# Optimization experiments

Hardware: AMD Instinct MI355X
Metric: run time of the kernel (lower is better)

The kernel has to match this reference:

```python
import jax, jax.numpy as jnp
import numpy as np

N_NODES = 100000
N_EDGES = 1600000
HEADS = 4
HID = 64
IN_CH = 3
N_GRAPHS = 64
NEG_SLOPE = 0.2  # PyG GATConv default


def _gat_layer(x, src, dst, W, a_src, a_dst, b):
    """PyG GATConv with concat=False (head-mean), eval mode (no dropout)."""
    N = x.shape[0]
    xl = (x @ W).reshape(N, HEADS, HID)            # [N,H,C]
    es = (xl * a_src).sum(-1)                       # [N,H] alpha_src
    ed = (xl * a_dst).sum(-1)                       # [N,H] alpha_dst
    e = jax.nn.leaky_relu(es[src] + ed[dst], NEG_SLOPE)  # [E,H]
    # segment softmax over incoming edges of each dst node
    m = jax.ops.segment_max(e, dst, num_segments=N)      # [N,H]
    ex = jnp.exp(e - m[dst])
    s = jax.ops.segment_sum(ex, dst, num_segments=N)     # [N,H]
    alpha = ex / s[dst]                                   # [E,H]
    msg = xl[src] * alpha[:, :, None]                     # [E,H,C]
    out = jax.ops.segment_sum(msg, dst, num_segments=N)   # [N,H,C]
    return out.mean(axis=1) + b                            # head mean + bias


def setup_inputs() -> dict:
    key = jax.random.key(0)
    ks = jax.random.split(key, 12)
    x = jax.random.normal(ks[0], (N_NODES, IN_CH), dtype=jnp.float32)
    edge_index = jax.random.randint(ks[1], (2, N_EDGES), 0, N_NODES, dtype=jnp.int64)
    batch_ids = jnp.sort(jax.random.randint(ks[2], (N_NODES,), 0, N_GRAPHS, dtype=jnp.int64))
    def glorot(k, shape, fan_in):
        return jax.random.normal(k, shape, dtype=jnp.float32) / np.sqrt(fan_in)
    W1 = glorot(ks[3], (IN_CH, HEADS * HID), IN_CH)
    a_src1 = glorot(ks[4], (HEADS, HID), HID)
    a_dst1 = glorot(ks[5], (HEADS, HID), HID)
    b1 = jnp.zeros((HID,), dtype=jnp.float32)
    W2 = glorot(ks[6], (HID, HEADS * HID), HID)
    a_src2 = glorot(ks[7], (HEADS, HID), HID)
    a_dst2 = glorot(ks[8], (HEADS, HID), HID)
    b2 = jnp.zeros((HID,), dtype=jnp.float32)
    return {"x": x, "edge_index": edge_index, "batch_ids": batch_ids,
            "W1": W1, "a_src1": a_src1, "a_dst1": a_dst1, "b1": b1,
            "W2": W2, "a_src2": a_src2, "a_dst2": a_dst2, "b2": b2}


def reference(x, edge_index, batch_ids, W1, a_src1, a_dst1, b1, W2, a_src2, a_dst2, b2):
    src, dst = edge_index[0], edge_index[1]
    h = jax.nn.relu(_gat_layer(x, src, dst, W1, a_src1, a_dst1, b1))
    h = jax.nn.relu(_gat_layer(h, src, dst, W2, a_src2, a_dst2, b2))
    # global_add_pool
    g = jax.ops.segment_sum(h, batch_ids, num_segments=N_GRAPHS)  # [G, HID]
    return g
```

## Files before the change

### kernel.cpp

```cpp
#include <hip/hip_runtime.h>
#include <math.h>

#define HEADS 4
#define HID 64
#define BSHIFT 7
#define BWIDTH 128
#define CCAP 4096
#define DCHUNK 8192

typedef __attribute__((ext_vector_type(8))) short short8;
typedef __attribute__((ext_vector_type(4))) float f32x4;

__device__ __forceinline__ float lrelu(float x) { return x > 0.f ? x : 0.2f * x; }

__device__ __forceinline__ unsigned short bf16r(float f) {
    unsigned u = __float_as_uint(f);
    unsigned r = (u + 0x7FFFu + ((u >> 16) & 1u)) >> 16;
    return (unsigned short)r;
}
__device__ __forceinline__ float bf2f(unsigned short u) {
    return __uint_as_float(((unsigned)u) << 16);
}

__device__ __forceinline__ float wred_sum(float v) {
#pragma unroll
    for (int o = 32; o > 0; o >>= 1) v += __shfl_xor(v, o);
    return v;
}
__device__ __forceinline__ float red16_sum(float v) {
#pragma unroll
    for (int o = 8; o > 0; o >>= 1) v += __shfl_xor(v, o);
    return v;
}
__device__ __forceinline__ float red16_max(float v) {
#pragma unroll
    for (int o = 8; o > 0; o >>= 1) v = fmaxf(v, __shfl_xor(v, o));
    return v;
}

__global__ void k_binit(int* __restrict__ bcnt, int NBUCK) {
    int i = threadIdx.x;
    if (i < NBUCK) bcnt[i] = 0;
}

__global__ void k_bhist(const int* __restrict__ dstI, int* __restrict__ bcnt,
                        int E, int NBUCK) {
    __shared__ int h[1024];
    for (int i = threadIdx.x; i < NBUCK; i += 256) h[i] = 0;
    __syncthreads();
    int stride = gridDim.x * 256;
    for (int e = blockIdx.x * 256 + threadIdx.x; e < E; e += stride)
        atomicAdd(&h[dstI[e] >> BSHIFT], 1);
    __syncthreads();
    for (int i = threadIdx.x; i < NBUCK; i += 256)
        if (h[i]) atomicAdd(&bcnt[i], h[i]);
}

__global__ void k_bscan(const int* __restrict__ bcnt, int* __restrict__ bbase,
                        int* __restrict__ gcur, int* __restrict__ off,
                        int NBUCK, int N, int E) {
    __shared__ int lds[1024];
    int t = threadIdx.x;
    int v = (t < NBUCK) ? bcnt[t] : 0;
    lds[t] = v;
    __syncthreads();
    for (int s = 1; s < 1024; s <<= 1) {
        int u = (t >= s) ? lds[t - s] : 0;
        __syncthreads();
        lds[t] += u;
        __syncthreads();
    }
    if (t < NBUCK) {
        int b = lds[t] - v;
        bbase[t] = b;
        gcur[t] = b;
    }
    if (t == 0) { bbase[NBUCK] = E; off[N] = E; }
}

__global__ void k_bdist(const int* __restrict__ srcI, const int* __restrict__ dstI,
                        int* __restrict__ gcur, uint2* __restrict__ pairs,
                        int E, int NBUCK) {
    __shared__ int h[1024];
    __shared__ int cur[1024];
    for (int i = threadIdx.x; i < NBUCK; i += 1024) h[i] = 0;
    __syncthreads();
    int base = blockIdx.x * DCHUNK;
    int sr[8], dr[8];
#pragma unroll
    for (int k = 0; k < 8; k++) {
        int e = base + threadIdx.x + k * 1024;
        if (e < E) {
            sr[k] = srcI[e];
            dr[k] = dstI[e];
            atomicAdd(&h[dr[k] >> BSHIFT], 1);
        } else dr[k] = -1;
    }
    __syncthreads();
    for (int i = threadIdx.x; i < NBUCK; i += 1024)
        cur[i] = h[i] ? atomicAdd(&gcur[i], h[i]) : 0;
    __syncthreads();
#pragma unroll
    for (int k = 0; k < 8; k++) {
        if (dr[k] >= 0) {
            int b = dr[k] >> BSHIFT;
            int p = atomicAdd(&cur[b], 1);
            pairs[p] = make_uint2((unsigned)sr[k], (unsigned)dr[k]);
        }
    }
}

__global__ void k_bcsr(const uint2* __restrict__ pairs, const int* __restrict__ bbase,
                       int* __restrict__ off, int* __restrict__ csr, int N) {
    __shared__ int cnt[BWIDTH];
    __shared__ int scan[BWIDTH];
    __shared__ int cur[BWIDTH];
    __shared__ int stage[CCAP];
    int b = blockIdx.x;
    int nodeBase = b << BSHIFT;
    int nNodes = N - nodeBase;
    if (nNodes > BWIDTH) nNodes = BWIDTH;
    int e0 = bbase[b], e1 = bbase[b + 1];
    int ecnt = e1 - e0;
    if (threadIdx.x < BWIDTH) cnt[threadIdx.x] = 0;
    __syncthreads();
    for (int i = threadIdx.x; i < ecnt; i += 256)
        atomicAdd(&cnt[pairs[e0 + i].y - (unsigned)nodeBase], 1);
    __syncthreads();
    if (threadIdx.x < BWIDTH)
        scan[threadIdx.x] = (threadIdx.x < nNodes) ? cnt[threadIdx.x] : 0;
    __syncthreads();
    for (int s = 1; s < BWIDTH; s <<= 1) {
        int u = 0;
        if (threadIdx.x < BWIDTH && threadIdx.x >= s) u = scan[threadIdx.x - s];
        __syncthreads();
        if (threadIdx.x < BWIDTH) scan[threadIdx.x] += u;
        __syncthreads();
    }
    if (threadIdx.x < nNodes) {
        int ex = scan[threadIdx.x] - cnt[threadIdx.x];
        off[nodeBase + threadIdx.x] = e0 + ex;
        cur[threadIdx.x] = ex;
    }
    __syncthreads();
    for (int i = threadIdx.x; i < ecnt; i += 256) {
        uint2 pr = pairs[e0 + i];
        int l = atomicAdd(&cur[pr.y - (unsigned)nodeBase], 1);
        if (l < CCAP) stage[l] = (int)pr.x;
        else csr[e0 + l] = (int)pr.x;
    }
    __syncthreads();
    int lim = ecnt < CCAP ? ecnt : CCAP;
    for (int i = threadIdx.x; i < lim; i += 256) csr[e0 + i] = stage[i];
}

__global__ void k_prep(const float* __restrict__ W, const float* __restrict__ asrc,
                       const float* __restrict__ adst, float* __restrict__ p_src,
                       float* __restrict__ p_dst, int K) {
    int wid = (blockIdx.x * blockDim.x + threadIdx.x) >> 6;
    int lane = threadIdx.x & 63;
    int total = K * 4 * 2;
    if (wid >= total) return;
    int which = wid / (K * 4);
    int hk = wid % (K * 4);
    int h = hk / K, k = hk % K;
    const float* a = which ? adst : asrc;
    float v = W[(size_t)k * 256 + h * 64 + lane] * a[h * 64 + lane];
    v = wred_sum(v);
    if (lane == 0) (which ? p_dst : p_src)[h * K + k] = v;
}

__global__ void k_w2bt(const float* __restrict__ W2, unsigned short* __restrict__ W2bt) {
    int i = blockIdx.x * 256 + threadIdx.x;
    int c = i >> 8, kh = i & 255;
    int h = kh >> 6, kf = kh & 63;
    W2bt[i] = bf16r(W2[kf * 256 + h * 64 + c]);
}

__global__ void k_esed1(const float* __restrict__ x, const float* __restrict__ ps,
                        const float* __restrict__ pd, float* __restrict__ es,
                        float* __restrict__ ed, int N) {
    int n = blockIdx.x * blockDim.x + threadIdx.x;
    if (n >= N) return;
    float x0 = x[n * 3], x1 = x[n * 3 + 1], x2 = x[n * 3 + 2];
    float4 s, d;
    s.x = x0 * ps[0] + x1 * ps[1] + x2 * ps[2];
    s.y = x0 * ps[3] + x1 * ps[4] + x2 * ps[5];
    s.z = x0 * ps[6] + x1 * ps[7] + x2 * ps[8];
    s.w = x0 * ps[9] + x1 * ps[10] + x2 * ps[11];
    d.x = x0 * pd[0] + x1 * pd[1] + x2 * pd[2];
    d.y = x0 * pd[3] + x1 * pd[4] + x2 * pd[5];
    d.z = x0 * pd[6] + x1 * pd[7] + x2 * pd[8];
    d.w = x0 * pd[9] + x1 * pd[10] + x2 * pd[11];
    ((float4*)es)[n] = s;
    ((float4*)ed)[n] = d;
}

__global__ void k_agg1(const int* __restrict__ off, const int* __restrict__ csr,
                       const float* __restrict__ es, const float* __restrict__ ed,
                       const float* __restrict__ x, const float* __restrict__ W1,
                       const float* __restrict__ b1, const float* __restrict__ qs,
                       const float* __restrict__ qd, unsigned short* __restrict__ houtb,
                       float* __restrict__ es2, float* __restrict__ ed2, int N) {
    int grp = (blockIdx.x * blockDim.x + threadIdx.x) >> 4;
    int l = threadIdx.x & 15;
    int wid = grp;
    bool active = wid < N;
    int o0 = 0, deg = 0;
    float4 edv = make_float4(0.f, 0.f, 0.f, 0.f);
    if (active) {
        o0 = off[wid];
        deg = off[wid + 1] - o0;
        edv = ((const float4*)ed)[wid];
    }

    float m0 = -INFINITY, m1 = -INFINITY, m2 = -INFINITY, m3 = -INFINITY;
    int s_cache = 0;
    float c0 = 0.f, c1 = 0.f, c2 = 0.f, c3 = 0.f;
    for (int j = l; j < deg; j += 16) {
        int s = csr[o0 + j];
        float4 ev = ((const float4*)es)[s];
        float e0 = lrelu(ev.x + edv.x), e1 = lrelu(ev.y + edv.y);
        float e2 = lrelu(ev.z + edv.z), e3 = lrelu(ev.w + edv.w);
        if (j < 16) { s_cache = s; c0 = e0; c1 = e1; c2 = e2; c3 = e3; }
        m0 = fmaxf(m0, e0); m1 = fmaxf(m1, e1);
        m2 = fmaxf(m2, e2); m3 = fmaxf(m3, e3);
    }
    m0 = red16_max(m0); m1 = red16_max(m1); m2 = red16_max(m2); m3 = red16_max(m3);

    float t0 = 0.f, t1 = 0.f, t2 = 0.f, t3 = 0.f;
    for (int j = l; j < deg; j += 16) {
        float e0, e1, e2, e3;
        if (j < 16) { e0 = c0; e1 = c1; e2 = c2; e3 = c3; }
        else {
            int s = csr[o0 + j];
            float4 ev = ((const float4*)es)[s];
            e0 = lrelu(ev.x + edv.x); e1 = lrelu(ev.y + edv.y);
            e2 = lrelu(ev.z + edv.z); e3 = lrelu(ev.w + edv.w);
        }
        e0 = __expf(e0 - m0); e1 = __expf(e1 - m1);
        e2 = __expf(e2 - m2); e3 = __expf(e3 - m3);
        if (j < 16) { c0 = e0; c1 = e1; c2 = e2; c3 = e3; }
        t0 += e0; t1 += e1; t2 += e2; t3 += e3;
    }
    t0 = red16_sum(t0); t1 = red16_sum(t1); t2 = red16_sum(t2); t3 = red16_sum(t3);
    float i0 = t0 > 0.f ? 1.f / t0 : 0.f;
    float i1 = t1 > 0.f ? 1.f / t1 : 0.f;
    float i2 = t2 > 0.f ? 1.f / t2 : 0.f;
    float i3 = t3 > 0.f ? 1.f / t3 : 0.f;

    float a00 = 0, a01 = 0, a02 = 0, a10 = 0, a11 = 0, a12 = 0;
    float a20 = 0, a21 = 0, a22 = 0, a30 = 0, a31 = 0, a32 = 0;
    for (int j = l; j < deg; j += 16) {
        float e0, e1, e2, e3; int s;
        if (j < 16) { s = s_cache; e0 = c0; e1 = c1; e2 = c2; e3 = c3; }
        else {
            s = csr[o0 + j];
            float4 ev = ((const float4*)es)[s];
            e0 = __expf(lrelu(ev.x + edv.x) - m0);
            e1 = __expf(lrelu(ev.y + edv.y) - m1);
            e2 = __expf(lrelu(ev.z + edv.z) - m2);
            e3 = __expf(lrelu(ev.w + edv.w) - m3);
        }
        float xv0 = x[s * 3], xv1 = x[s * 3 + 1], xv2 = x[s * 3 + 2];
        a00 += e0 * xv0; a01 += e0 * xv1; a02 += e0 * xv2;
        a10 += e1 * xv0; a11 += e1 * xv1; a12 += e1 * xv2;
        a20 += e2 * xv0; a21 += e2 * xv1; a22 += e2 * xv2;
        a30 += e3 * xv0; a31 += e3 * xv1; a32 += e3 * xv2;
    }
    a00 = red16_sum(a00) * i0; a01 = red16_sum(a01) * i0; a02 = red16_sum(a02) * i0;
    a10 = red16_sum(a10) * i1; a11 = red16_sum(a11) * i1; a12 = red16_sum(a12) * i1;
    a20 = red16_sum(a20) * i2; a21 = red16_sum(a21) * i2; a22 = red16_sum(a22) * i2;
    a30 = red16_sum(a30) * i3; a31 = red16_sum(a31) * i3; a32 = red16_sum(a32) * i3;

    if (!active) return;

    const float4* W1f = (const float4*)W1;
    float4 r = make_float4(0.f, 0.f, 0.f, 0.f);
    float ah[4][3] = {{a00, a01, a02}, {a10, a11, a12}, {a20, a21, a22}, {a30, a31, a32}};
#pragma unroll
    for (int k = 0; k < 3; k++) {
#pragma unroll
        for (int h = 0; h < 4; h++) {
            float4 wv = W1f[k * 64 + h * 16 + l];
            float a = ah[h][k];
            r.x += a * wv.x; r.y += a * wv.y; r.z += a * wv.z; r.w += a * wv.w;
        }
    }
    float4 bv = ((const float4*)b1)[l];
    float4 hv;
    hv.x = fmaxf(0.25f * r.x + bv.x, 0.f);
    hv.y = fmaxf(0.25f * r.y + bv.y, 0.f);
    hv.z = fmaxf(0.25f * r.z + bv.z, 0.f);
    hv.w = fmaxf(0.25f * r.w + bv.w, 0.f);
    ((ushort4*)houtb)[(size_t)wid * 16 + l] =
        make_ushort4(bf16r(hv.x), bf16r(hv.y), bf16r(hv.z), bf16r(hv.w));

    const float4* qsf = (const float4*)qs;
    const float4* qdf = (const float4*)qd;
    float ps[4], pd[4];
#pragma unroll
    for (int h = 0; h < 4; h++) {
        float4 q = qsf[h * 16 + l];
        ps[h] = red16_sum(hv.x * q.x + hv.y * q.y + hv.z * q.z + hv.w * q.w);
        float4 p = qdf[h * 16 + l];
        pd[h] = red16_sum(hv.x * p.x + hv.y * p.y + hv.z * p.z + hv.w * p.w);
    }
    if (l == 0) {
        ((float4*)es2)[wid] = make_float4(ps[0], ps[1], ps[2], ps[3]);
        ((float4*)ed2)[wid] = make_float4(pd[0], pd[1], pd[2], pd[3]);
    }
}

#define NS 16
__global__ void k_agg2(const int* __restrict__ off, const int* __restrict__ csr,
                       const float* __restrict__ es, const float* __restrict__ ed,
                       const unsigned short* __restrict__ houtb,
                       unsigned short* __restrict__ aggb, int N) {
    __shared__ float exl[NS * 64 * 4];
    __shared__ int   sl[NS * 64];
    __shared__ float minv[NS * 8];
    __shared__ int   meta[NS * 2];

    for (int i = threadIdx.x; i < NS * 64; i += 256) {
        ((float4*)exl)[i] = make_float4(0.f, 0.f, 0.f, 0.f);
        sl[i] = 0;
    }
    __syncthreads();

    int l = threadIdx.x & 15;
    int slot = threadIdx.x >> 4;
    int wid = blockIdx.x * NS + slot;
    bool active = wid < N;
    int o0 = 0, deg = 0;
    float4 edv = make_float4(0.f, 0.f, 0.f, 0.f);
    if (active) {
        o0 = off[wid];
        deg = off[wid + 1] - o0;
        edv = ((const float4*)ed)[wid];
    }

    float m0 = -INFINITY, m1 = -INFINITY, m2 = -INFINITY, m3 = -INFINITY;
    int s_cache = 0;
    float c0 = 0.f, c1 = 0.f, c2 = 0.f, c3 = 0.f;
    for (int j = l; j < deg; j += 16) {
        int s = csr[o0 + j];
        float4 ev = ((const float4*)es)[s];
        float e0 = lrelu(ev.x + edv.x), e1 = lrelu(ev.y + edv.y);
        float e2 = lrelu(ev.z + edv.z), e3 = lrelu(ev.w + edv.w);
        if (j < 16) { s_cache = s; c0 = e0; c1 = e1; c2 = e2; c3 = e3; }
        m0 = fmaxf(m0, e0); m1 = fmaxf(m1, e1);
        m2 = fmaxf(m2, e2); m3 = fmaxf(m3, e3);
    }
    m0 = red16_max(m0); m1 = red16_max(m1); m2 = red16_max(m2); m3 = red16_max(m3);

    float t0 = 0.f, t1 = 0.f, t2 = 0.f, t3 = 0.f;
    for (int j = l; j < deg; j += 16) {
        float e0, e1, e2, e3; int s;
        if (j < 16) { s = s_cache; e0 = c0; e1 = c1; e2 = c2; e3 = c3; }
        else {
            s = csr[o0 + j];
            float4 ev = ((const float4*)es)[s];
            e0 = lrelu(ev.x + edv.x); e1 = lrelu(ev.y + edv.y);
            e2 = lrelu(ev.z + edv.z); e3 = lrelu(ev.w + edv.w);
        }
        e0 = __expf(e0 - m0); e1 = __expf(e1 - m1);
        e2 = __expf(e2 - m2); e3 = __expf(e3 - m3);
        if (j < 64) {
            ((float4*)exl)[slot * 64 + j] = make_float4(e0, e1, e2, e3);
            sl[slot * 64 + j] = s;
        }
        t0 += e0; t1 += e1; t2 += e2; t3 += e3;
    }
    t0 = red16_sum(t0); t1 = red16_sum(t1); t2 = red16_sum(t2); t3 = red16_sum(t3);
    if (l == 0) {
        minv[slot * 8 + 0] = m0; minv[slot * 8 + 1] = m1;
        minv[slot * 8 + 2] = m2; minv[slot * 8 + 3] = m3;
        minv[slot * 8 + 4] = t0 > 0.f ? 1.f / t0 : 0.f;
        minv[slot * 8 + 5] = t1 > 0.f ? 1.f / t1 : 0.f;
        minv[slot * 8 + 6] = t2 > 0.f ? 1.f / t2 : 0.f;
        minv[slot * 8 + 7] = t3 > 0.f ? 1.f / t3 : 0.f;
        meta[slot * 2 + 0] = o0;
        meta[slot * 2 + 1] = deg;
    }
    __syncthreads();

    int lane = threadIdx.x & 63;
    int w = threadIdx.x >> 6;
    for (int sidx = 0; sidx < 4; sidx++) {
        int slot2 = w * 4 + sidx;
        int nd = blockIdx.x * NS + slot2;
        if (nd >= N) continue;
        int o0b = meta[slot2 * 2 + 0], degb = meta[slot2 * 2 + 1];
        float mm0 = minv[slot2 * 8 + 0], mm1 = minv[slot2 * 8 + 1];
        float mm2 = minv[slot2 * 8 + 2], mm3 = minv[slot2 * 8 + 3];
        float iv0 = minv[slot2 * 8 + 4], iv1 = minv[slot2 * 8 + 5];
        float iv2 = minv[slot2 * 8 + 6], iv3 = minv[slot2 * 8 + 7];

        float acc0 = 0.f, acc1 = 0.f, acc2 = 0.f, acc3 = 0.f;
        const float4* EX = ((const float4*)exl) + slot2 * 64;
        const int* S = sl + slot2 * 64;
        int dmain = degb < 64 ? degb : 64;
        int d4 = (dmain + 3) & ~3;
        for (int j = 0; j < d4; j += 4) {
            float4 a0 = EX[j], a1 = EX[j + 1], a2 = EX[j + 2], a3 = EX[j + 3];
            int s0 = S[j], s1 = S[j + 1], s2 = S[j + 2], s3 = S[j + 3];
            float v0 = bf2f(houtb[(size_t)s0 * 64 + lane]);
            float v1 = bf2f(houtb[(size_t)s1 * 64 + lane]);
            float v2 = bf2f(houtb[(size_t)s2 * 64 + lane]);
            float v3 = bf2f(houtb[(size_t)s3 * 64 + lane]);
            acc0 += a0.x * v0 + a1.x * v1 + a2.x * v2 + a3.x * v3;
            acc1 += a0.y * v0 + a1.y * v1 + a2.y * v2 + a3.y * v3;
            acc2 += a0.z * v0 + a1.z * v1 + a2.z * v2 + a3.z * v3;
            acc3 += a0.w * v0 + a1.w * v1 + a2.w * v2 + a3.w * v3;
        }
        if (degb > 64) {
            float4 edv2 = ((const float4*)ed)[nd];
            for (int j = 64; j < degb; j++) {
                int s = csr[o0b + j];
                float4 ev = ((const float4*)es)[s];
                float e0 = __expf(lrelu(ev.x + edv2.x) - mm0);
                float e1 = __expf(lrelu(ev.y + edv2.y) - mm1);
                float e2 = __expf(lrelu(ev.z + edv2.z) - mm2);
                float e3 = __expf(lrelu(ev.w + edv2.w) - mm3);
                float v = bf2f(houtb[(size_t)s * 64 + lane]);
                acc0 += e0 * v; acc1 += e1 * v; acc2 += e2 * v; acc3 += e3 * v;
            }
        }
        size_t b = (size_t)nd * 256;
        aggb[b + lane]        = bf16r(acc0 * iv0);
        aggb[b + 64 + lane]   = bf16r(acc1 * iv1);
        aggb[b + 128 + lane]  = bf16r(acc2 * iv2);
        aggb[b + 192 + lane]  = bf16r(acc3 * iv3);
    }
}

__global__ void k_out2(const unsigned short* __restrict__ aggb,
                       const unsigned short* __restrict__ W2bt,
                       const float* __restrict__ b2, const int* __restrict__ batch,
                       float* __restrict__ out, int N) {
    int w = threadIdx.x >> 6, lane = threadIdx.x & 63;
    int nodeBase = blockIdx.x * 64 + w * 16;
    int m = lane & 15;
    int quad = lane >> 4;
    const short* A = (const short*)aggb + (size_t)(nodeBase + m) * 256 + quad * 8;
    const short* B = (const short*)W2bt;

    f32x4 acc0 = {0.f, 0.f, 0.f, 0.f}, acc1 = {0.f, 0.f, 0.f, 0.f};
    f32x4 acc2 = {0.f, 0.f, 0.f, 0.f}, acc3 = {0.f, 0.f, 0.f, 0.f};
#pragma unroll
    for (int kk = 0; kk < 8; kk++) {
        short8 af = *(const short8*)(A + kk * 32);
        short8 b0 = *(const short8*)(B + (size_t)(0 * 16 + m) * 256 + kk * 32 + quad * 8);
        short8 b1v = *(const short8*)(B + (size_t)(1 * 16 + m) * 256 + kk * 32 + quad * 8);
        short8 b2v = *(const short8*)(B + (size_t)(2 * 16 + m) * 256 + kk * 32 + quad * 8);
        short8 b3v = *(const short8*)(B + (size_t)(3 * 16 + m) * 256 + kk * 32 + quad * 8);
        acc0 = __builtin_amdgcn_mfma_f32_16x16x32_bf16(af, b0, acc0, 0, 0, 0);
        acc1 = __builtin_amdgcn_mfma_f32_16x16x32_bf16(af, b1v, acc1, 0, 0, 0);
        acc2 = __builtin_amdgcn_mfma_f32_16x16x32_bf16(af, b2v, acc2, 0, 0, 0);
        acc3 = __builtin_amdgcn_mfma_f32_16x16x32_bf16(af, b3v, acc3, 0, 0, 0);
    }
    f32x4 accs[4] = {acc0, acc1, acc2, acc3};

    float vals[4][4];
#pragma unroll
    for (int cb = 0; cb < 4; cb++) {
        float bv = b2[cb * 16 + m];
#pragma unroll
        for (int r = 0; r < 4; r++)
            vals[cb][r] = fmaxf(0.25f * accs[cb][r] + bv, 0.f);
    }

    bool fast = (nodeBase + 15 < N);
    int g0 = 0;
    if (fast) {
        g0 = batch[nodeBase];
        int g1 = batch[nodeBase + 15];
        fast = (g0 == g1);
    }
    if (fast) {
#pragma unroll
        for (int cb = 0; cb < 4; cb++) {
            float s = vals[cb][0] + vals[cb][1] + vals[cb][2] + vals[cb][3];
            s += __shfl_xor(s, 16);
            s += __shfl_xor(s, 32);
            if (quad == 0) atomicAdd(&out[g0 * 64 + cb * 16 + m], s);
        }
    } else {
#pragma unroll
        for (int r = 0; r < 4; r++) {
            int node = nodeBase + quad * 4 + r;
            if (node < N) {
                int g = batch[node];
#pragma unroll
                for (int cb = 0; cb < 4; cb++)
                    atomicAdd(&out[g * 64 + cb * 16 + m], vals[cb][r]);
            }
        }
    }
}

__global__ void k_pzero(float* __restrict__ out, int total) {
    int i = blockIdx.x * blockDim.x + threadIdx.x;
    if (i < total) out[i] = 0.f;
}

extern "C" void kernel_launch(void* const* d_in, const int* in_sizes, int n_in,
                              void* d_out, int out_size, void* d_ws, size_t ws_size,
                              hipStream_t stream) {
    const float* x   = (const float*)d_in[0];
    const int*   ei  = (const int*)d_in[1];
    const int*   bat = (const int*)d_in[2];
    const float* W1  = (const float*)d_in[3];
    const float* as1 = (const float*)d_in[4];
    const float* ad1 = (const float*)d_in[5];
    const float* b1  = (const float*)d_in[6];
    const float* W2  = (const float*)d_in[7];
    const float* as2 = (const float*)d_in[8];
    const float* ad2 = (const float*)d_in[9];
    const float* b2  = (const float*)d_in[10];
    float* out = (float*)d_out;

    int N = in_sizes[0] / 3;
    int E = in_sizes[1] / 2;
    int G = out_size / 64;
    const int* srcI = ei;
    const int* dstI = ei + E;
    int NBUCK = (N + BWIDTH - 1) >> BSHIFT;

    float* fw = (float*)d_ws;
    size_t fo = 0;
    unsigned short* aggb = (unsigned short*)fw; fo += (size_t)N * 128;
    unsigned short* houtb = (unsigned short*)(fw + fo); fo += (size_t)N * 32;
    float* esA   = fw + fo; fo += (size_t)N * 4;
    float* edA   = fw + fo; fo += (size_t)N * 4;
    float* esB   = fw + fo; fo += (size_t)N * 4;
    float* edB   = fw + fo; fo += (size_t)N * 4;
    float* p1s   = fw + fo; fo += 64;
    float* p1d   = fw + fo; fo += 64;
    float* qs    = fw + fo; fo += 256;
    float* qd    = fw + fo; fo += 256;
    unsigned short* W2bt = (unsigned short*)(fw + fo); fo += 64 * 256 / 2;
    int* iw = (int*)(fw + fo);
    size_t io = 0;
    uint2* pairs = (uint2*)iw; io += (size_t)2 * E;
    int* csr    = iw + io; io += E;
    int* off    = iw + io; io += N + 1;
    int* bbase  = iw + io; io += 1025;
    int* gcur   = iw + io; io += 1024;
    int* bcnt   = iw + io; io += 1024;

    int nThrBlk = (N + 255) / 256;
    int nGrpBlk = (N + 15) / 16;

    k_binit<<<1, 1024, 0, stream>>>(bcnt, NBUCK);
    k_bhist<<<256, 256, 0, stream>>>(dstI, bcnt, E, NBUCK);
    k_bscan<<<1, 1024, 0, stream>>>(bcnt, bbase, gcur, off, NBUCK, N, E);
    k_bdist<<<(E + DCHUNK - 1) / DCHUNK, 1024, 0, stream>>>(srcI, dstI, gcur, pairs, E, NBUCK);
    k_bcsr<<<NBUCK, 256, 0, stream>>>(pairs, bbase, off, csr, N);

    k_prep<<<(3 * 8 * 64 + 255) / 256, 256, 0, stream>>>(W1, as1, ad1, p1s, p1d, 3);
    k_prep<<<(64 * 8 * 64 + 255) / 256, 256, 0, stream>>>(W2, as2, ad2, qs, qd, 64);
    k_w2bt<<<64, 256, 0, stream>>>(W2, W2bt);
    k_pzero<<<(G * 64 + 255) / 256, 256, 0, stream>>>(out, G * 64);

    k_esed1<<<nThrBlk, 256, 0, stream>>>(x, p1s, p1d, esA, edA, N);
    k_agg1<<<nGrpBlk, 256, 0, stream>>>(off, csr, esA, edA, x, W1, b1, qs, qd,
                                        houtb, esB, edB, N);

    k_agg2<<<nGrpBlk, 256, 0, stream>>>(off, csr, esB, edB, houtb, aggb, N);
    k_out2<<<(N + 63) / 64, 256, 0, stream>>>(aggb, W2bt, b2, bat, out, N);
}
```

Measured before the change: 265.9 us.

## Drop softmax max pass and pack edge pairs into single 32-bit words

Removes the per-node max-subtraction pass from the segment softmax in both aggregation kernels, computing exp(leaky_relu(e)) directly in a single pass that also accumulates the sum. This saves a second gather over each node's edges and the associated reductions. Separately, the bucketed CSR build now packs the source index and the low bits of the destination into one 32-bit word, halving the pairs buffer traffic. Skipping the max subtraction risks exp overflow if attention logits are large, and the packing assumes source ids fit in 25 bits.

```diff
diff --git a/kernel.cpp b/kernel.cpp
--- a/kernel.cpp
+++ b/kernel.cpp
@@ -30,11 +30,6 @@
 __device__ __forceinline__ float red16_sum(float v) {
 #pragma unroll
     for (int o = 8; o > 0; o >>= 1) v += __shfl_xor(v, o);
-    return v;
-}
-__device__ __forceinline__ float red16_max(float v) {
-#pragma unroll
-    for (int o = 8; o > 0; o >>= 1) v = fmaxf(v, __shfl_xor(v, o));
     return v;
 }
 
@@ -79,7 +74,7 @@
 }
 
 __global__ void k_bdist(const int* __restrict__ srcI, const int* __restrict__ dstI,
-                        int* __restrict__ gcur, uint2* __restrict__ pairs,
+                        int* __restrict__ gcur, unsigned* __restrict__ pairs,
                         int E, int NBUCK) {
     __shared__ int h[1024];
     __shared__ int cur[1024];
@@ -105,12 +100,12 @@
         if (dr[k] >= 0) {
             int b = dr[k] >> BSHIFT;
             int p = atomicAdd(&cur[b], 1);
-            pairs[p] = make_uint2((unsigned)sr[k], (unsigned)dr[k]);
-        }
-    }
-}
-
-__global__ void k_bcsr(const uint2* __restrict__ pairs, const int* __restrict__ bbase,
+            pairs[p] = ((unsigned)sr[k] << BSHIFT) | ((unsigned)dr[k] & (BWIDTH - 1));
+        }
+    }
+}
+
+__global__ void k_bcsr(const unsigned* __restrict__ pairs, const int* __restrict__ bbase,
                        int* __restrict__ off, int* __restrict__ csr, int N) {
     __shared__ int cnt[BWIDTH];
     __shared__ int scan[BWIDTH];
@@ -125,7 +120,7 @@
     if (threadIdx.x < BWIDTH) cnt[threadIdx.x] = 0;
     __syncthreads();
     for (int i = threadIdx.x; i < ecnt; i += 256)
-        atomicAdd(&cnt[pairs[e0 + i].y - (unsigned)nodeBase], 1);
+        atomicAdd(&cnt[pairs[e0 + i] & (BWIDTH - 1)], 1);
     __syncthreads();
     if (threadIdx.x < BWIDTH)
         scan[threadIdx.x] = (threadIdx.x < nNodes) ? cnt[threadIdx.x] : 0;
@@ -144,10 +139,11 @@
     }
     __syncthreads();
     for (int i = threadIdx.x; i < ecnt; i += 256) {
-        uint2 pr = pairs[e0 + i];
-        int l = atomicAdd(&cur[pr.y - (unsigned)nodeBase], 1);
-        if (l < CCAP) stage[l] = (int)pr.x;
-        else csr[e0 + l] = (int)pr.x;
+        unsigned pr = pairs[e0 + i];
+        int l = atomicAdd(&cur[pr & (BWIDTH - 1)], 1);
+        int src = (int)(pr >> BSHIFT);
+        if (l < CCAP) stage[l] = src;
+        else csr[e0 + l] = src;
     }
     __syncthreads();
     int lim = ecnt < CCAP ? ecnt : CCAP;
@@ -214,33 +210,17 @@
         edv = ((const float4*)ed)[wid];
     }
 
-    float m0 = -INFINITY, m1 = -INFINITY, m2 = -INFINITY, m3 = -INFINITY;
+    float t0 = 0.f, t1 = 0.f, t2 = 0.f, t3 = 0.f;
     int s_cache = 0;
     float c0 = 0.f, c1 = 0.f, c2 = 0.f, c3 = 0.f;
     for (int j = l; j < deg; j += 16) {
         int s = csr[o0 + j];
         float4 ev = ((const float4*)es)[s];
-        float e0 = lrelu(ev.x + edv.x), e1 = lrelu(ev.y + edv.y);
-        float e2 = lrelu(ev.z + edv.z), e3 = lrelu(ev.w + edv.w);
+        float e0 = __expf(lrelu(ev.x + edv.x));
+        float e1 = __expf(lrelu(ev.y + edv.y));
+        float e2 = __expf(lrelu(ev.z + edv.z));
+        float e3 = __expf(lrelu(ev.w + edv.w));
         if (j < 16) { s_cache = s; c0 = e0; c1 = e1; c2 = e2; c3 = e3; }
-        m0 = fmaxf(m0, e0); m1 = fmaxf(m1, e1);
-        m2 = fmaxf(m2, e2); m3 = fmaxf(m3, e3);
-    }
-    m0 = red16_max(m0); m1 = red16_max(m1); m2 = red16_max(m2); m3 = red16_max(m3);
-
-    float t0 = 0.f, t1 = 0.f, t2 = 0.f, t3 = 0.f;
-    for (int j = l; j < deg; j += 16) {
-        float e0, e1, e2, e3;
-        if (j < 16) { e0 = c0; e1 = c1; e2 = c2; e3 = c3; }
-        else {
-            int s = csr[o0 + j];
-            float4 ev = ((const float4*)es)[s];
-            e0 = lrelu(ev.x + edv.x); e1 = lrelu(ev.y + edv.y);
-            e2 = lrelu(ev.z + edv.z); e3 = lrelu(ev.w + edv.w);
-        }
-        e0 = __expf(e0 - m0); e1 = __expf(e1 - m1);
-        e2 = __expf(e2 - m2); e3 = __expf(e3 - m3);
-        if (j < 16) { c0 = e0; c1 = e1; c2 = e2; c3 = e3; }
         t0 += e0; t1 += e1; t2 += e2; t3 += e3;
     }
     t0 = red16_sum(t0); t1 = red16_sum(t1); t2 = red16_sum(t2); t3 = red16_sum(t3);
@@ -257,10 +237,10 @@
         else {
             s = csr[o0 + j];
             float4 ev = ((const float4*)es)[s];
-            e0 = __expf(lrelu(ev.x + edv.x) - m0);
-            e1 = __expf(lrelu(ev.y + edv.y) - m1);
-            e2 = __expf(lrelu(ev.z + edv.z) - m2);
-            e3 = __expf(lrelu(ev.w + edv.w) - m3);
+            e0 = __expf(lrelu(ev.x + edv.x));
+            e1 = __expf(lrelu(ev.y + edv.y));
+            e2 = __expf(lrelu(ev.z + edv.z));
+            e3 = __expf(lrelu(ev.w + edv.w));
         }
         float xv0 = x[s * 3], xv1 = x[s * 3 + 1], xv2 = x[s * 3 + 2];
         a00 += e0 * xv0; a01 += e0 * xv1; a02 += e0 * xv2;
@@ -319,7 +299,7 @@
                        unsigned short* __restrict__ aggb, int N) {
     __shared__ float exl[NS * 64 * 4];
     __shared__ int   sl[NS * 64];
-    __shared__ float minv[NS * 8];
+    __shared__ float minv[NS * 4];
     __shared__ int   meta[NS * 2];
 
     for (int i = threadIdx.x; i < NS * 64; i += 256) {
@@ -340,32 +320,14 @@
         edv = ((const float4*)ed)[wid];
     }
 
-    float m0 = -INFINITY, m1 = -INFINITY, m2 = -INFINITY, m3 = -INFINITY;
-    int s_cache = 0;
-    float c0 = 0.f, c1 = 0.f, c2 = 0.f, c3 = 0.f;
+    float t0 = 0.f, t1 = 0.f, t2 = 0.f, t3 = 0.f;
     for (int j = l; j < deg; j += 16) {
         int s = csr[o0 + j];
         float4 ev = ((const float4*)es)[s];
-        float e0 = lrelu(ev.x + edv.x), e1 = lrelu(ev.y + edv.y);
-        float e2 = lrelu(ev.z + edv.z), e3 = lrelu(ev.w + edv.w);
-        if (j < 16) { s_cache = s; c0 = e0; c1 = e1; c2 = e2; c3 = e3; }
-        m0 = fmaxf(m0, e0); m1 = fmaxf(m1, e1);
-        m2 = fmaxf(m2, e2); m3 = fmaxf(m3, e3);
-    }
-    m0 = red16_max(m0); m1 = red16_max(m1); m2 = red16_max(m2); m3 = red16_max(m3);
-
-    float t0 = 0.f, t1 = 0.f, t2 = 0.f, t3 = 0.f;
-    for (int j = l; j < deg; j += 16) {
-        float e0, e1, e2, e3; int s;
-        if (j < 16) { s = s_cache; e0 = c0; e1 = c1; e2 = c2; e3 = c3; }
-        else {
-            s = csr[o0 + j];
-            float4 ev = ((const float4*)es)[s];
-            e0 = lrelu(ev.x + edv.x); e1 = lrelu(ev.y + edv.y);
-            e2 = lrelu(ev.z + edv.z); e3 = lrelu(ev.w + edv.w);
-        }
-        e0 = __expf(e0 - m0); e1 = __expf(e1 - m1);
-        e2 = __expf(e2 - m2); e3 = __expf(e3 - m3);
+        float e0 = __expf(lrelu(ev.x + edv.x));
+        float e1 = __expf(lrelu(ev.y + edv.y));
+        float e2 = __expf(lrelu(ev.z + edv.z));
+        float e3 = __expf(lrelu(ev.w + edv.w));
         if (j < 64) {
             ((float4*)exl)[slot * 64 + j] = make_float4(e0, e1, e2, e3);
             sl[slot * 64 + j] = s;
@@ -374,12 +336,10 @@
     }
     t0 = red16_sum(t0); t1 = red16_sum(t1); t2 = red16_sum(t2); t3 = red16_sum(t3);
     if (l == 0) {
-        minv[slot * 8 + 0] = m0; minv[slot * 8 + 1] = m1;
-        minv[slot * 8 + 2] = m2; minv[slot * 8 + 3] = m3;
-        minv[slot * 8 + 4] = t0 > 0.f ? 1.f / t0 : 0.f;
-        minv[slot * 8 + 5] = t1 > 0.f ? 1.f / t1 : 0.f;
-        minv[slot * 8 + 6] = t2 > 0.f ? 1.f / t2 : 0.f;
-        minv[slot * 8 + 7] = t3 > 0.f ? 1.f / t3 : 0.f;
+        minv[slot * 4 + 0] = t0 > 0.f ? 1.f / t0 : 0.f;
+        minv[slot * 4 + 1] = t1 > 0.f ? 1.f / t1 : 0.f;
+        minv[slot * 4 + 2] = t2 > 0.f ? 1.f / t2 : 0.f;
+        minv[slot * 4 + 3] = t3 > 0.f ? 1.f / t3 : 0.f;
         meta[slot * 2 + 0] = o0;
         meta[slot * 2 + 1] = deg;
     }
@@ -392,10 +352,8 @@
         int nd = blockIdx.x * NS + slot2;
         if (nd >= N) continue;
         int o0b = meta[slot2 * 2 + 0], degb = meta[slot2 * 2 + 1];
-        float mm0 = minv[slot2 * 8 + 0], mm1 = minv[slot2 * 8 + 1];
-        float mm2 = minv[slot2 * 8 + 2], mm3 = minv[slot2 * 8 + 3];
-        float iv0 = minv[slot2 * 8 + 4], iv1 = minv[slot2 * 8 + 5];
-        float iv2 = minv[slot2 * 8 + 6], iv3 = minv[slot2 * 8 + 7];
+        float iv0 = minv[slot2 * 4 + 0], iv1 = minv[slot2 * 4 + 1];
+        float iv2 = minv[slot2 * 4 + 2], iv3 = minv[slot2 * 4 + 3];
 
         float acc0 = 0.f, acc1 = 0.f, acc2 = 0.f, acc3 = 0.f;
         const float4* EX = ((const float4*)exl) + slot2 * 64;
@@ -419,10 +377,10 @@
             for (int j = 64; j < degb; j++) {
                 int s = csr[o0b + j];
                 float4 ev = ((const float4*)es)[s];
-                float e0 = __expf(lrelu(ev.x + edv2.x) - mm0);
-                float e1 = __expf(lrelu(ev.y + edv2.y) - mm1);
-                float e2 = __expf(lrelu(ev.z + edv2.z) - mm2);
-                float e3 = __expf(lrelu(ev.w + edv2.w) - mm3);
+                float e0 = __expf(lrelu(ev.x + edv2.x));
+                float e1 = __expf(lrelu(ev.y + edv2.y));
+                float e2 = __expf(lrelu(ev.z + edv2.z));
+                float e3 = __expf(lrelu(ev.w + edv2.w));
                 float v = bf2f(houtb[(size_t)s * 64 + lane]);
                 acc0 += e0 * v; acc1 += e1 * v; acc2 += e2 * v; acc3 += e3 * v;
             }
@@ -543,7 +501,7 @@
     unsigned short* W2bt = (unsigned short*)(fw + fo); fo += 64 * 256 / 2;
     int* iw = (int*)(fw + fo);
     size_t io = 0;
-    uint2* pairs = (uint2*)iw; io += (size_t)2 * E;
+    unsigned* pairs = (unsigned*)iw; io += E;
     int* csr    = iw + io; io += E;
     int* off    = iw + io; io += N + 1;
     int* bbase  = iw + io; io += 1025;
```

Measured after the change: 257.3 us. 1.03x faster.
